# Performance work log

Hardware: AMD Instinct MI355X
Metric: run time of the kernel (lower is better)

The kernel has to match this reference:

```python
import jax, jax.numpy as jnp
import numpy as np

HEADS = 16
DIM_HEAD = 64
SCALE = float(np.sqrt(DIM_HEAD))  # NOTE: original code MULTIPLIES by sqrt(dim_head)


def setup_inputs() -> dict:
    key = jax.random.key(0)
    k1, k2, k3, k4 = jax.random.split(key, 4)
    dim = 1024
    b, n = 2, 2048
    s = 1.0 / np.sqrt(dim)
    return {
        "x": jax.random.normal(k1, (b, n, dim), dtype=jnp.float32),
        "w_q": jax.random.normal(k2, (dim, HEADS * DIM_HEAD), dtype=jnp.float32) * s,
        "w_vk": jax.random.normal(k3, (dim, HEADS * DIM_HEAD * 2), dtype=jnp.float32) * s,
        "w_out": jax.random.normal(k4, (HEADS * DIM_HEAD, dim), dtype=jnp.float32) * s,
    }


def reference(x, w_q, w_vk, w_out):
    b, n, _ = x.shape
    h, d = HEADS, DIM_HEAD
    context = x  # context=None, kv_include_self=False
    q = (x @ w_q).reshape(b, n, h, d).transpose(0, 2, 1, 3)          # b h n d
    kv = context @ w_vk                                              # b n 2hd
    k, v = jnp.split(kv, 2, axis=-1)                                 # chunk order: k first, v second
    k = k.reshape(b, n, h, d).transpose(0, 2, 1, 3)
    v = v.reshape(b, n, h, d).transpose(0, 2, 1, 3)
    dots = jnp.einsum('bhid,bhjd->bhij', q, k) * SCALE               # faithful: multiply by sqrt(d)
    attn = jax.nn.softmax(dots, axis=-1)                             # dropout p=0 -> identity
    out = jnp.einsum('bhij,bhjd->bhid', attn, v)
    out = out.transpose(0, 2, 1, 3).reshape(b, n, h * d)
    return out @ w_out
```

## Files before the change

kernel.cpp:

```cpp
#include <hip/hip_runtime.h>

typedef _Float16 half4 __attribute__((ext_vector_type(4)));
typedef _Float16 half8 __attribute__((ext_vector_type(8)));
typedef _Float16 h2pk __attribute__((ext_vector_type(2)));
typedef float f32x4 __attribute__((ext_vector_type(4)));

#define MFMA_F16K32(a, b, c) __builtin_amdgcn_mfma_f32_16x16x32_f16(a, b, c, 0, 0, 0)
#define MFMA_F16K16(a, b, c) __builtin_amdgcn_mfma_f32_16x16x16f16(a, b, c, 0, 0, 0)
#define EXP2F(x) __builtin_amdgcn_exp2f(x)
#define CVT_PK(a, b) __builtin_bit_cast(h2pk, __builtin_amdgcn_cvt_pkrtz(a, b))

constexpr int NSEQ = 2048, DIM = 1024;
constexpr float QSCALE = 11.5415603271f;

__device__ __forceinline__ void ld_lds16(void* lds, const void* g) {
  __builtin_amdgcn_global_load_lds(
      (const __attribute__((address_space(1))) void*)g,
      (__attribute__((address_space(3))) void*)lds, 16, 0, 0);
}

__global__ __launch_bounds__(256) void prep(
    const float* __restrict__ w_q, const float* __restrict__ w_vk,
    const float* __restrict__ w_out, const float* __restrict__ x,
    _Float16* __restrict__ WT, _Float16* __restrict__ WoT,
    _Float16* __restrict__ xf) {
  const int bid = blockIdx.x;
  const int t = threadIdx.x;
  if (bid >= 1024) {
    const size_t i = ((size_t)(bid - 1024) * 256 + t) * 8;
    float4 a = *(const float4*)(x + i), b2 = *(const float4*)(x + i + 4);
    float v[8] = {a.x, a.y, a.z, a.w, b2.x, b2.y, b2.z, b2.w};
    half8 h;
#pragma unroll
    for (int j = 0; j < 8; ++j) h[j] = (_Float16)v[j];
    *(half8*)(xf + i) = h;
    return;
  }
  __shared__ float T[64][65];
  const int bx = bid & 63, k0 = (bid >> 6) * 64;
  const float* src;
  int srcN, n0, dstrow, mode;
  float scale;
  if (bx < 16) {
    src = w_q; srcN = 1024; n0 = bx * 64; dstrow = n0; scale = QSCALE; mode = 0;
  } else if (bx < 48) {
    src = w_vk; srcN = 2048; n0 = (bx - 16) * 64; dstrow = 1024 + n0;
    scale = 1.0f; mode = 0;
  } else {
    src = w_out; srcN = 1024; n0 = (bx - 48) * 64; dstrow = n0;
    scale = 1.0f; mode = 1;
  }
  {
    const int r = t >> 2, c4 = (t & 3) * 16;
    const float* s = src + (size_t)(k0 + r) * srcN + n0 + c4;
    float4 v0 = ((const float4*)s)[0], v1 = ((const float4*)s)[1],
           v2 = ((const float4*)s)[2], v3 = ((const float4*)s)[3];
    *(float4*)&T[r][c4 + 0] = v0;  *(float4*)&T[r][c4 + 4] = v1;
    *(float4*)&T[r][c4 + 8] = v2;  *(float4*)&T[r][c4 + 12] = v3;
  }
  __syncthreads();
  const int rn = t >> 2, kc = (t & 3) * 16;
  half8 hv[2];
#pragma unroll
  for (int half = 0; half < 2; ++half)
#pragma unroll
    for (int j = 0; j < 8; ++j)
      hv[half][j] = (_Float16)(T[kc + half * 8 + j][rn] * scale);
  _Float16* d = ((mode == 0) ? WT + (size_t)(dstrow + rn) * 1024
                             : WoT + (size_t)(n0 + rn) * 1024) + k0 + kc;
  *(half8*)d = hv[0]; *(half8*)(d + 8) = hv[1];
}

__global__ __launch_bounds__(256, 3) void proj6(
    const _Float16* __restrict__ xf, const _Float16* __restrict__ WT,
    _Float16* __restrict__ qb, _Float16* __restrict__ kb,
    _Float16* __restrict__ VT) {
  __shared__ __align__(16) char smem[32768];
  const int t = threadIdx.x;
  const int lane = t & 63, wave = t >> 6, quad = lane >> 4, lq = lane & 15;
  const int bn = blockIdx.x * 128, bm = blockIdx.y * 128;
  const int kind = bn >> 10;
  const int wm = (wave >> 1) * 64, wn = (wave & 1) * 64;

  const int srow = lane >> 2;
  const int schk = (lane & 3) ^ (srow & 3);
  const _Float16* xg = xf + (size_t)(bm + wave * 32 + srow) * DIM + schk * 8;
  const _Float16* bg = WT + (size_t)(bn + wave * 32 + srow) * DIM + schk * 8;
  const int wb = wave * 2048;

  auto issue = [&](char* buf, int k0) {
    ld_lds16(buf + wb,                xg + k0);
    ld_lds16(buf + wb + 1024,         xg + k0 + 16 * DIM);
    ld_lds16(buf + 8192 + wb,         bg + k0);
    ld_lds16(buf + 8192 + wb + 1024,  bg + k0 + 16 * DIM);
  };

  const int swz = (quad ^ (lq & 3)) * 8;

  f32x4 acc[4][4];
#pragma unroll
  for (int i = 0; i < 4; ++i)
#pragma unroll
    for (int j = 0; j < 4; ++j) acc[i][j] = (f32x4){0.f, 0.f, 0.f, 0.f};

  char* bufA = smem;
  char* bufB = smem + 16384;
  issue(bufA, 0);
  for (int k0 = 0; k0 < DIM; k0 += 32) {
    char* cur = ((k0 >> 5) & 1) ? bufB : bufA;
    char* nxt = ((k0 >> 5) & 1) ? bufA : bufB;
    __syncthreads();
    if (k0 + 32 < DIM) issue(nxt, k0 + 32);
    const _Float16* Xs = (const _Float16*)cur;
    const _Float16* Bs = (const _Float16*)(cur + 8192);
    half8 ah[4];
#pragma unroll
    for (int i = 0; i < 4; ++i)
      ah[i] = *(const half8*)&Xs[(wm + i * 16 + lq) * 32 + swz];
#pragma unroll
    for (int j = 0; j < 4; ++j) {
      half8 bf = *(const half8*)&Bs[(wn + j * 16 + lq) * 32 + swz];
#pragma unroll
      for (int i = 0; i < 4; ++i) acc[i][j] = MFMA_F16K32(ah[i], bf, acc[i][j]);
    }
  }

  if (kind == 2) {
#pragma unroll
    for (int i = 0; i < 4; ++i)
#pragma unroll
      for (int j = 0; j < 4; ++j) {
        const int c = (bn - 2048) + wn + j * 16 + lq;
        const int row0 = bm + wm + i * 16 + quad * 4;
        const int b = row0 >> 11, n = row0 & 2047;
        const int h = c >> 6, d = c & 63;
        half4 o;
#pragma unroll
        for (int r = 0; r < 4; ++r) o[r] = (_Float16)acc[i][j][r];
        *(half4*)(VT + ((size_t)(b * 16 + h) * 64 + d) * 2048 + n) = o;
      }
  } else {
    _Float16* D = (kind == 0) ? qb : kb;
    const int cb = bn & 1023;
#pragma unroll
    for (int i = 0; i < 4; ++i)
#pragma unroll
      for (int j = 0; j < 4; ++j) {
        const int col = cb + wn + j * 16 + lq;
#pragma unroll
        for (int r = 0; r < 4; ++r) {
          const int row = bm + wm + i * 16 + quad * 4 + r;
          D[(size_t)row * 1024 + col] = (_Float16)acc[i][j][r];
        }
      }
  }
}

__global__ __launch_bounds__(512, 4) void attn8(
    const _Float16* __restrict__ qb, const _Float16* __restrict__ kb,
    const _Float16* __restrict__ vT, _Float16* __restrict__ ho) {
  __shared__ __align__(16) char smem[65536];
  const int t = threadIdx.x;
  const int lane = t & 63, wave = t >> 6, quad = lane >> 4, lq = lane & 15;
  const int group = wave >> 2, wq = wave & 3;
  const int i0 = blockIdx.x * 128;
  const int bh = blockIdx.y, b = bh >> 4, head = bh & 15;
  const size_t rowbase = (size_t)b * NSEQ;

  half8 qf[2][2];
#pragma unroll
  for (int qt = 0; qt < 2; ++qt) {
    const _Float16* qp =
        qb + (rowbase + i0 + wq * 32 + qt * 16 + lq) * DIM + head * 64 + quad * 8;
    qf[qt][0] = *(const half8*)qp;
    qf[qt][1] = *(const half8*)(qp + 32);
  }

  f32x4 o[2][4];
#pragma unroll
  for (int qt = 0; qt < 2; ++qt)
#pragma unroll
    for (int dt = 0; dt < 4; ++dt) o[qt][dt] = (f32x4){0.f, 0.f, 0.f, 0.f};
  float mrun[2] = {-3.0e38f, -3.0e38f};
  float lrun[2] = {0.f, 0.f};

  const int srow = lane >> 3, schk = (lane & 7) ^ srow;
  const _Float16* kgp =
      kb + (rowbase + wq * 16 + srow) * DIM + head * 64 + schk * 8;
  const _Float16* vgp =
      vT + ((size_t)bh * 64 + wq * 16 + srow) * 2048 + schk * 8;

  auto issue = [&](int bsel, int j) {
    char* kd = smem + (group * 2 + bsel) * 8192 + wq * 2048;
    char* vd = kd + 32768;
    ld_lds16(kd,        kgp + (size_t)j * DIM);
    ld_lds16(kd + 1024, kgp + (size_t)(j + 8) * DIM);
    ld_lds16(vd,        vgp + j);
    ld_lds16(vd + 1024, vgp + 8 * 2048 + j);
  };

  const int swzK0 = (quad ^ (lq & 7)) * 8;
  const int swzK1 = ((quad + 4) ^ (lq & 7)) * 8;

  issue(0, group * 64);

  for (int p = 0; p < 16; ++p) {
    const int cur = p & 1;
    __syncthreads();
    if (p < 15) issue(cur ^ 1, (2 * p + group) * 64 + 128);
    const _Float16* Khs = (const _Float16*)(smem + (group * 2 + cur) * 8192);
    const _Float16* Vts = (const _Float16*)(smem + 32768 + (group * 2 + cur) * 8192);

    f32x4 s[2][4];
    __builtin_amdgcn_s_setprio(1);
#pragma unroll
    for (int nt = 0; nt < 4; ++nt) {
      const int roff = (nt * 16 + lq) * 64;
      half8 k0f = *(const half8*)&Khs[roff + swzK0];
      half8 k1f = *(const half8*)&Khs[roff + swzK1];
#pragma unroll
      for (int qt = 0; qt < 2; ++qt) {
        f32x4 sv = (f32x4){0.f, 0.f, 0.f, 0.f};
        sv = MFMA_F16K32(k0f, qf[qt][0], sv);
        sv = MFMA_F16K32(k1f, qf[qt][1], sv);
        s[qt][nt] = sv;
      }
    }
    __builtin_amdgcn_s_setprio(0);

    half4 pbv[2][4];
#pragma unroll
    for (int qt = 0; qt < 2; ++qt) {
      float m0 = fmaxf(fmaxf(s[qt][0][0], s[qt][0][1]),
                       fmaxf(s[qt][0][2], s[qt][0][3]));
      float m1 = fmaxf(fmaxf(s[qt][1][0], s[qt][1][1]),
                       fmaxf(s[qt][1][2], s[qt][1][3]));
      float m2 = fmaxf(fmaxf(s[qt][2][0], s[qt][2][1]),
                       fmaxf(s[qt][2][2], s[qt][2][3]));
      float m3 = fmaxf(fmaxf(s[qt][3][0], s[qt][3][1]),
                       fmaxf(s[qt][3][2], s[qt][3][3]));
      float mx = fmaxf(fmaxf(m0, m1), fmaxf(m2, m3));
      mx = fmaxf(mx, __shfl_xor(mx, 16));
      mx = fmaxf(mx, __shfl_xor(mx, 32));
      const float mn = fmaxf(mrun[qt], mx);
      const float alpha = EXP2F(mrun[qt] - mn);
      mrun[qt] = mn;
      float rs = 0.f;
#pragma unroll
      for (int nt = 0; nt < 4; ++nt) {
        float p0 = EXP2F(s[qt][nt][0] - mn), p1 = EXP2F(s[qt][nt][1] - mn);
        float p2 = EXP2F(s[qt][nt][2] - mn), p3 = EXP2F(s[qt][nt][3] - mn);
        rs += (p0 + p1) + (p2 + p3);
        h2pk lo = CVT_PK(p0, p1);
        h2pk hi = CVT_PK(p2, p3);
        pbv[qt][nt] = (half4){lo[0], lo[1], hi[0], hi[1]};
      }
      rs += __shfl_xor(rs, 16);
      rs += __shfl_xor(rs, 32);
      lrun[qt] = lrun[qt] * alpha + rs;
#pragma unroll
      for (int dt = 0; dt < 4; ++dt) o[qt][dt] *= alpha;
    }

    __builtin_amdgcn_s_setprio(1);
#pragma unroll
    for (int dt = 0; dt < 4; ++dt) {
      const int vrow = (dt * 16 + lq) * 64;
#pragma unroll
      for (int ntj = 0; ntj < 4; ++ntj) {
        const int voff =
            vrow + (((2 * ntj + (quad >> 1)) ^ (lq & 7)) * 8) + (quad & 1) * 4;
        half4 va = *(const half4*)&Vts[voff];
        o[0][dt] = MFMA_F16K16(va, pbv[0][ntj], o[0][dt]);
        o[1][dt] = MFMA_F16K16(va, pbv[1][ntj], o[1][dt]);
      }
    }
    __builtin_amdgcn_s_setprio(0);
  }

  float* dump = (float*)smem;
  __syncthreads();
  if (group == 1) {
    float* D = dump + wq * 2304 + lane * 36;
#pragma unroll
    for (int qt = 0; qt < 2; ++qt)
#pragma unroll
      for (int dt = 0; dt < 4; ++dt)
        *(f32x4*)(D + (qt * 4 + dt) * 4) = o[qt][dt];
    D[32] = mrun[0]; D[33] = lrun[0]; D[34] = mrun[1]; D[35] = lrun[1];
  }
  __syncthreads();
  _Float16* Ots = (_Float16*)(smem + 40960);
  if (group == 0) {
    const float* D = dump + wq * 2304 + lane * 36;
#pragma unroll
    for (int qt = 0; qt < 2; ++qt) {
      const float m2 = D[32 + qt * 2], l2 = D[33 + qt * 2];
      const float mM = fmaxf(mrun[qt], m2);
      const float f1 = EXP2F(mrun[qt] - mM);
      const float f2 = EXP2F(m2 - mM);
      const float inv = 1.0f / (lrun[qt] * f1 + l2 * f2);
#pragma unroll
      for (int dt = 0; dt < 4; ++dt) {
        f32x4 o2 = *(const f32x4*)(D + (qt * 4 + dt) * 4);
#pragma unroll
        for (int r = 0; r < 4; ++r) {
          const float val = (o[qt][dt][r] * f1 + o2[r] * f2) * inv;
          Ots[(wq * 32 + qt * 16 + lq) * 80 + dt * 16 + quad * 4 + r] =
              (_Float16)val;
        }
      }
    }
  }
  __syncthreads();
  {
    const int row = t >> 2, seg = t & 3;
    const _Float16* src = &Ots[row * 80 + seg * 16];
    half8 o0 = ((const half8*)src)[0], o1 = ((const half8*)src)[1];
    _Float16* dst = ho + (rowbase + i0 + row) * DIM + head * 64 + seg * 16;
    ((half8*)dst)[0] = o0; ((half8*)dst)[1] = o1;
  }
}

__global__ __launch_bounds__(256, 4) void gemm_out(
    const _Float16* __restrict__ A, const _Float16* __restrict__ BT,
    float* __restrict__ C) {
  __shared__ __align__(16) char smem[24576];
  const int t = threadIdx.x;
  const int lane = t & 63, wave = t >> 6, quad = lane >> 4, lq = lane & 15;
  const int bn = blockIdx.x * 128, bm = blockIdx.y * 64;
  const int wm = (wave >> 1) * 32, wn = (wave & 1) * 64;

  const int bco = (lane & 7) ^ (lane >> 3);
  const int brow = 2 * (lane >> 3) + (bco >> 2);
  const int bcc = bco & 3;
  const _Float16* ag = A + (size_t)(bm + wave * 16 + brow) * DIM + bcc * 8;
  const _Float16* bg = BT + (size_t)(bn + wave * 32 + brow) * DIM + bcc * 8;
  const int swzB = ((((lq & 1) << 2) | quad) ^ ((lq >> 1) & 7)) * 8;

  auto issue = [&](char* buf, int k0) {
    ld_lds16(buf + wave * 1024,               ag + k0);
    ld_lds16(buf + 4096 + wave * 2048,        bg + k0);
    ld_lds16(buf + 4096 + wave * 2048 + 1024, bg + k0 + 16 * DIM);
  };

  f32x4 acc[2][4];
#pragma unroll
  for (int i = 0; i < 2; ++i)
#pragma unroll
    for (int j = 0; j < 4; ++j) acc[i][j] = (f32x4){0.f, 0.f, 0.f, 0.f};

  char* bufA = smem;
  char* bufB = smem + 12288;
  issue(bufA, 0);
  for (int k0 = 0; k0 < DIM; k0 += 32) {
    char* cur = ((k0 >> 5) & 1) ? bufB : bufA;
    char* nxt = ((k0 >> 5) & 1) ? bufA : bufB;
    __syncthreads();
    if (k0 + 32 < DIM) issue(nxt, k0 + 32);
    const _Float16* Ahs = (const _Float16*)cur;
    const _Float16* Bhs = (const _Float16*)(cur + 4096);
    half8 ah[2];
#pragma unroll
    for (int i = 0; i < 2; ++i) {
      const int row = wm + i * 16 + lq;
      ah[i] = *(const half8*)&Ahs[(row >> 1) * 64 + swzB];
    }
#pragma unroll
    for (int j = 0; j < 4; ++j) {
      const int row = wn + j * 16 + lq;
      half8 bf = *(const half8*)&Bhs[(row >> 1) * 64 + swzB];
#pragma unroll
      for (int i = 0; i < 2; ++i) acc[i][j] = MFMA_F16K32(ah[i], bf, acc[i][j]);
    }
  }
#pragma unroll
  for (int i = 0; i < 2; ++i)
#pragma unroll
    for (int j = 0; j < 4; ++j) {
      const int col = bn + wn + j * 16 + lq;
#pragma unroll
      for (int r = 0; r < 4; ++r) {
        const int row = bm + wm + i * 16 + quad * 4 + r;
        C[(size_t)row * 1024 + col] = acc[i][j][r];
      }
    }
}

extern "C" void kernel_launch(void* const* d_in, const int* in_sizes, int n_in,
                              void* d_out, int out_size, void* d_ws,
                              size_t ws_size, hipStream_t stream) {
  const float* x     = (const float*)d_in[0];
  const float* w_q   = (const float*)d_in[1];
  const float* w_vk  = (const float*)d_in[2];
  const float* w_out = (const float*)d_in[3];
  float* out = (float*)d_out;

  char* w = (char*)d_ws;
  _Float16* wT  = (_Float16*)(w);
  _Float16* woT = (_Float16*)(w + (6ull << 20));
  _Float16* qbb = (_Float16*)(w + (8ull << 20));
  _Float16* kbb = (_Float16*)(w + (16ull << 20));
  _Float16* vTb = (_Float16*)(w + (24ull << 20));
  _Float16* hob = (_Float16*)(w + (32ull << 20));
  _Float16* xfb = (_Float16*)(w + (40ull << 20));

  dim3 blk(256);
  prep<<<dim3(3072), blk, 0, stream>>>(w_q, w_vk, w_out, x, wT, woT, xfb);
  proj6<<<dim3(24, 32), blk, 0, stream>>>(xfb, wT, qbb, kbb, vTb);
  attn8<<<dim3(16, 32), dim3(512), 0, stream>>>(qbb, kbb, vTb, hob);
  gemm_out<<<dim3(8, 64), blk, 0, stream>>>(hob, woT, out);
}
```

Measured before the change: 189.1 us.

## Stage V-transpose stores via LDS, lazy softmax rescale, larger output GEMM tiles

The V-projection epilogue now stages each tile through shared memory so the transposed V writes go out as contiguous 16-byte chunks instead of scattered half4 stores. The attention kernel precomputes its LDS offsets and skips the running-max rescale unless the max has grown by more than a threshold, which removes exps and multiplies from most iterations. The output GEMM moves from 64x128 to 128x128 tiles with the same swizzled layout as the projection kernel, raising data reuse at the cost of occupancy (3 blocks per CU) and half as many blocks. The lazy rescale lets exp2 arguments exceed zero, up to 2^8 in fp16 probabilities, which carries a small overflow and accuracy risk.

```diff
diff --git a/kernel.cpp b/kernel.cpp
--- a/kernel.cpp
+++ b/kernel.cpp
@@ -62,10 +62,10 @@
   const int rn = t >> 2, kc = (t & 3) * 16;
   half8 hv[2];
 #pragma unroll
-  for (int half = 0; half < 2; ++half)
+  for (int hh = 0; hh < 2; ++hh)
 #pragma unroll
     for (int j = 0; j < 8; ++j)
-      hv[half][j] = (_Float16)(T[kc + half * 8 + j][rn] * scale);
+      hv[hh][j] = (_Float16)(T[kc + hh * 8 + j][rn] * scale);
   _Float16* d = ((mode == 0) ? WT + (size_t)(dstrow + rn) * 1024
                              : WoT + (size_t)(n0 + rn) * 1024) + k0 + kc;
   *(half8*)d = hv[0]; *(half8*)(d + 8) = hv[1];
@@ -126,19 +126,40 @@
   }
 
   if (kind == 2) {
-#pragma unroll
-    for (int i = 0; i < 4; ++i)
-#pragma unroll
-      for (int j = 0; j < 4; ++j) {
-        const int c = (bn - 2048) + wn + j * 16 + lq;
-        const int row0 = bm + wm + i * 16 + quad * 4;
-        const int b = row0 >> 11, n = row0 & 2047;
-        const int h = c >> 6, d = c & 63;
-        half4 o;
-#pragma unroll
-        for (int r = 0; r < 4; ++r) o[r] = (_Float16)acc[i][j][r];
-        *(half4*)(VT + ((size_t)(b * 16 + h) * 64 + d) * 2048 + n) = o;
-      }
+    _Float16* Ols = (_Float16*)smem;
+    const int cb = bn - 2048;
+    __syncthreads();
+#pragma unroll
+    for (int pass = 0; pass < 2; ++pass) {
+      if ((wave >> 1) == pass) {
+#pragma unroll
+        for (int i = 0; i < 4; ++i)
+#pragma unroll
+          for (int j = 0; j < 4; ++j) {
+            const int c = wn + j * 16 + lq;
+            const int tl = i * 16 + quad * 4;
+            half4 o;
+#pragma unroll
+            for (int r = 0; r < 4; ++r) o[r] = (_Float16)acc[i][j][r];
+            *(half4*)&Ols[c * 68 + tl] = o;
+          }
+      }
+      __syncthreads();
+      {
+        const int c = t >> 1, hf = t & 1;
+        const int gcol = cb + c;
+        const int tok0 = bm + pass * 64 + hf * 32;
+        const int b2 = tok0 >> 11, n2 = tok0 & 2047;
+        const _Float16* src = &Ols[c * 68 + hf * 32];
+        half8 v0 = ((const half8*)src)[0], v1 = ((const half8*)src)[1],
+              v2 = ((const half8*)src)[2], v3 = ((const half8*)src)[3];
+        _Float16* dst =
+            VT + ((size_t)(b2 * 16 + (gcol >> 6)) * 64 + (gcol & 63)) * 2048 + n2;
+        ((half8*)dst)[0] = v0; ((half8*)dst)[1] = v1;
+        ((half8*)dst)[2] = v2; ((half8*)dst)[3] = v3;
+      }
+      __syncthreads();
+    }
   } else {
     _Float16* D = (kind == 0) ? qb : kb;
     const int cb = bn & 1023;
@@ -202,6 +223,21 @@
   const int swzK0 = (quad ^ (lq & 7)) * 8;
   const int swzK1 = ((quad + 4) ^ (lq & 7)) * 8;
 
+  int koffs[4][2];
+#pragma unroll
+  for (int nt = 0; nt < 4; ++nt) {
+    koffs[nt][0] = (nt * 16 + lq) * 64 + swzK0;
+    koffs[nt][1] = (nt * 16 + lq) * 64 + swzK1;
+  }
+  int voffs[4][4];
+#pragma unroll
+  for (int dt = 0; dt < 4; ++dt)
+#pragma unroll
+    for (int ntj = 0; ntj < 4; ++ntj)
+      voffs[dt][ntj] = (dt * 16 + lq) * 64 +
+                       (((2 * ntj + (quad >> 1)) ^ (lq & 7)) * 8) +
+                       (quad & 1) * 4;
+
   issue(0, group * 64);
 
   for (int p = 0; p < 16; ++p) {
@@ -215,9 +251,8 @@
     __builtin_amdgcn_s_setprio(1);
 #pragma unroll
     for (int nt = 0; nt < 4; ++nt) {
-      const int roff = (nt * 16 + lq) * 64;
-      half8 k0f = *(const half8*)&Khs[roff + swzK0];
-      half8 k1f = *(const half8*)&Khs[roff + swzK1];
+      half8 k0f = *(const half8*)&Khs[koffs[nt][0]];
+      half8 k1f = *(const half8*)&Khs[koffs[nt][1]];
 #pragma unroll
       for (int qt = 0; qt < 2; ++qt) {
         f32x4 sv = (f32x4){0.f, 0.f, 0.f, 0.f};
@@ -231,25 +266,29 @@
     half4 pbv[2][4];
 #pragma unroll
     for (int qt = 0; qt < 2; ++qt) {
-      float m0 = fmaxf(fmaxf(s[qt][0][0], s[qt][0][1]),
-                       fmaxf(s[qt][0][2], s[qt][0][3]));
-      float m1 = fmaxf(fmaxf(s[qt][1][0], s[qt][1][1]),
-                       fmaxf(s[qt][1][2], s[qt][1][3]));
-      float m2 = fmaxf(fmaxf(s[qt][2][0], s[qt][2][1]),
-                       fmaxf(s[qt][2][2], s[qt][2][3]));
-      float m3 = fmaxf(fmaxf(s[qt][3][0], s[qt][3][1]),
-                       fmaxf(s[qt][3][2], s[qt][3][3]));
-      float mx = fmaxf(fmaxf(m0, m1), fmaxf(m2, m3));
+      float t0 = fmaxf(fmaxf(s[qt][0][0], s[qt][0][1]), s[qt][0][2]);
+      float t1 = fmaxf(fmaxf(s[qt][0][3], s[qt][1][0]), s[qt][1][1]);
+      float t2 = fmaxf(fmaxf(s[qt][1][2], s[qt][1][3]), s[qt][2][0]);
+      float t3 = fmaxf(fmaxf(s[qt][2][1], s[qt][2][2]), s[qt][2][3]);
+      float t4 = fmaxf(fmaxf(s[qt][3][0], s[qt][3][1]), s[qt][3][2]);
+      float mx = fmaxf(fmaxf(fmaxf(t0, t1), t2),
+                       fmaxf(fmaxf(t3, t4), s[qt][3][3]));
       mx = fmaxf(mx, __shfl_xor(mx, 16));
       mx = fmaxf(mx, __shfl_xor(mx, 32));
-      const float mn = fmaxf(mrun[qt], mx);
-      const float alpha = EXP2F(mrun[qt] - mn);
-      mrun[qt] = mn;
+      if (!__all(mx - mrun[qt] <= 8.0f)) {
+        const float mn = fmaxf(mrun[qt], mx);
+        const float alpha = EXP2F(mrun[qt] - mn);
+        mrun[qt] = mn;
+        lrun[qt] *= alpha;
+#pragma unroll
+        for (int dt = 0; dt < 4; ++dt) o[qt][dt] *= alpha;
+      }
+      const float mn2 = mrun[qt];
       float rs = 0.f;
 #pragma unroll
       for (int nt = 0; nt < 4; ++nt) {
-        float p0 = EXP2F(s[qt][nt][0] - mn), p1 = EXP2F(s[qt][nt][1] - mn);
-        float p2 = EXP2F(s[qt][nt][2] - mn), p3 = EXP2F(s[qt][nt][3] - mn);
+        float p0 = EXP2F(s[qt][nt][0] - mn2), p1 = EXP2F(s[qt][nt][1] - mn2);
+        float p2 = EXP2F(s[qt][nt][2] - mn2), p3 = EXP2F(s[qt][nt][3] - mn2);
         rs += (p0 + p1) + (p2 + p3);
         h2pk lo = CVT_PK(p0, p1);
         h2pk hi = CVT_PK(p2, p3);
@@ -257,20 +296,15 @@
       }
       rs += __shfl_xor(rs, 16);
       rs += __shfl_xor(rs, 32);
-      lrun[qt] = lrun[qt] * alpha + rs;
-#pragma unroll
-      for (int dt = 0; dt < 4; ++dt) o[qt][dt] *= alpha;
+      lrun[qt] += rs;
     }
 
     __builtin_amdgcn_s_setprio(1);
 #pragma unroll
     for (int dt = 0; dt < 4; ++dt) {
-      const int vrow = (dt * 16 + lq) * 64;
 #pragma unroll
       for (int ntj = 0; ntj < 4; ++ntj) {
-        const int voff =
-            vrow + (((2 * ntj + (quad >> 1)) ^ (lq & 7)) * 8) + (quad & 1) * 4;
-        half4 va = *(const half4*)&Vts[voff];
+        half4 va = *(const half4*)&Vts[voffs[dt][ntj]];
         o[0][dt] = MFMA_F16K16(va, pbv[0][ntj], o[0][dt]);
         o[1][dt] = MFMA_F16K16(va, pbv[1][ntj], o[1][dt]);
       }
@@ -322,36 +356,38 @@
   }
 }
 
-__global__ __launch_bounds__(256, 4) void gemm_out(
+__global__ __launch_bounds__(256, 3) void gemm_out(
     const _Float16* __restrict__ A, const _Float16* __restrict__ BT,
     float* __restrict__ C) {
-  __shared__ __align__(16) char smem[24576];
+  __shared__ __align__(16) char smem[32768];
   const int t = threadIdx.x;
   const int lane = t & 63, wave = t >> 6, quad = lane >> 4, lq = lane & 15;
-  const int bn = blockIdx.x * 128, bm = blockIdx.y * 64;
-  const int wm = (wave >> 1) * 32, wn = (wave & 1) * 64;
-
-  const int bco = (lane & 7) ^ (lane >> 3);
-  const int brow = 2 * (lane >> 3) + (bco >> 2);
-  const int bcc = bco & 3;
-  const _Float16* ag = A + (size_t)(bm + wave * 16 + brow) * DIM + bcc * 8;
-  const _Float16* bg = BT + (size_t)(bn + wave * 32 + brow) * DIM + bcc * 8;
-  const int swzB = ((((lq & 1) << 2) | quad) ^ ((lq >> 1) & 7)) * 8;
+  const int bn = blockIdx.x * 128, bm = blockIdx.y * 128;
+  const int wm = (wave >> 1) * 64, wn = (wave & 1) * 64;
+
+  const int srow = lane >> 2;
+  const int schk = (lane & 3) ^ (srow & 3);
+  const _Float16* ag = A + (size_t)(bm + wave * 32 + srow) * DIM + schk * 8;
+  const _Float16* bg = BT + (size_t)(bn + wave * 32 + srow) * DIM + schk * 8;
+  const int wb = wave * 2048;
 
   auto issue = [&](char* buf, int k0) {
-    ld_lds16(buf + wave * 1024,               ag + k0);
-    ld_lds16(buf + 4096 + wave * 2048,        bg + k0);
-    ld_lds16(buf + 4096 + wave * 2048 + 1024, bg + k0 + 16 * DIM);
+    ld_lds16(buf + wb,                ag + k0);
+    ld_lds16(buf + wb + 1024,         ag + k0 + 16 * DIM);
+    ld_lds16(buf + 8192 + wb,         bg + k0);
+    ld_lds16(buf + 8192 + wb + 1024,  bg + k0 + 16 * DIM);
   };
 
-  f32x4 acc[2][4];
-#pragma unroll
-  for (int i = 0; i < 2; ++i)
+  const int swz = (quad ^ (lq & 3)) * 8;
+
+  f32x4 acc[4][4];
+#pragma unroll
+  for (int i = 0; i < 4; ++i)
 #pragma unroll
     for (int j = 0; j < 4; ++j) acc[i][j] = (f32x4){0.f, 0.f, 0.f, 0.f};
 
   char* bufA = smem;
-  char* bufB = smem + 12288;
+  char* bufB = smem + 16384;
   issue(bufA, 0);
   for (int k0 = 0; k0 < DIM; k0 += 32) {
     char* cur = ((k0 >> 5) & 1) ? bufB : bufA;
@@ -359,23 +395,20 @@
     __syncthreads();
     if (k0 + 32 < DIM) issue(nxt, k0 + 32);
     const _Float16* Ahs = (const _Float16*)cur;
-    const _Float16* Bhs = (const _Float16*)(cur + 4096);
-    half8 ah[2];
-#pragma unroll
-    for (int i = 0; i < 2; ++i) {
-      const int row = wm + i * 16 + lq;
-      ah[i] = *(const half8*)&Ahs[(row >> 1) * 64 + swzB];
-    }
+    const _Float16* Bhs = (const _Float16*)(cur + 8192);
+    half8 ah[4];
+#pragma unroll
+    for (int i = 0; i < 4; ++i)
+      ah[i] = *(const half8*)&Ahs[(wm + i * 16 + lq) * 32 + swz];
 #pragma unroll
     for (int j = 0; j < 4; ++j) {
-      const int row = wn + j * 16 + lq;
-      half8 bf = *(const half8*)&Bhs[(row >> 1) * 64 + swzB];
-#pragma unroll
-      for (int i = 0; i < 2; ++i) acc[i][j] = MFMA_F16K32(ah[i], bf, acc[i][j]);
-    }
-  }
-#pragma unroll
-  for (int i = 0; i < 2; ++i)
+      half8 bf = *(const half8*)&Bhs[(wn + j * 16 + lq) * 32 + swz];
+#pragma unroll
+      for (int i = 0; i < 4; ++i) acc[i][j] = MFMA_F16K32(ah[i], bf, acc[i][j]);
+    }
+  }
+#pragma unroll
+  for (int i = 0; i < 4; ++i)
 #pragma unroll
     for (int j = 0; j < 4; ++j) {
       const int col = bn + wn + j * 16 + lq;
@@ -409,5 +442,5 @@
   prep<<<dim3(3072), blk, 0, stream>>>(w_q, w_vk, w_out, x, wT, woT, xfb);
   proj6<<<dim3(24, 32), blk, 0, stream>>>(xfb, wT, qbb, kbb, vTb);
   attn8<<<dim3(16, 32), dim3(512), 0, stream>>>(qbb, kbb, vTb, hob);
-  gemm_out<<<dim3(8, 64), blk, 0, stream>>>(hob, woT, out);
-}
+  gemm_out<<<dim3(8, 32), blk, 0, stream>>>(hob, woT, out);
+}
```

Measured after the change: 188.7 us. About the same (-0.2%).
